# Performance work log

Hardware: AMD Instinct MI355X
Metric: run time of the kernel (lower is better)

Reference implementation:

```python
import jax, jax.numpy as jnp
import numpy as np

GAMMA = 2.0
CONTEXT_WINDOW = 100


def setup_inputs() -> dict:
    key = jax.random.key(0)
    k1, k2 = jax.random.split(key)
    B, S, C = 64, 131072, 3
    inputs = jax.random.normal(k1, (B, S, C), dtype=jnp.float32)
    targets = jax.random.randint(k2, (B, S), 0, C, dtype=jnp.int32)
    alpha = jnp.array([0.25, 1.0, 1.0], dtype=jnp.float32)
    return {"inputs": inputs, "targets": targets, "alpha": alpha}


def _window_mask(targets, window):
    # mask[b, i] = True iff any positive target within +/- window of i;
    # rows with no positives are fully True (matches torch loop semantics).
    B, S = targets.shape
    pos = targets > 0                                   # (B, S) bool
    cs = jnp.cumsum(pos.astype(jnp.int32), axis=1)      # inclusive prefix sums
    c = jnp.concatenate([jnp.zeros((B, 1), jnp.int32), cs], axis=1)  # (B, S+1)
    idx = jnp.arange(S)
    hi = jnp.minimum(idx + window + 1, S)               # exclusive end
    lo = jnp.maximum(idx - window, 0)                   # inclusive start
    count = c[:, hi] - c[:, lo]                         # positives in window
    mask = count > 0
    has_pos = pos.any(axis=1, keepdims=True)
    return jnp.where(has_pos, mask, True)


def reference(inputs, targets, alpha):
    # inputs: (B, S, C) logits; targets: (B, S) class indices
    mask = _window_mask(targets, CONTEXT_WINDOW)                     # (B, S)
    logp = jax.nn.log_softmax(inputs, axis=-1)                       # (B, S, C)
    ce = -jnp.take_along_axis(logp, targets[..., None].astype(jnp.int32), axis=-1)[..., 0]
    p_t = jnp.exp(-ce)
    focal = alpha[targets] * (1.0 - p_t) ** GAMMA * ce               # (B, S)
    m = mask.astype(inputs.dtype)
    # masked mean == mean over selected elements in the torch version
    return jnp.sum(focal * m) / jnp.sum(m)
```

## Files before the change

### kernel.cpp

```cpp
#include <hip/hip_runtime.h>

#define BB 64
#define SS 131072
#define CC 3
#define WIN 100
#define TILE 2048
#define NTHREADS 256
#define NBLOCKS (BB * (SS / TILE))
#define EXT (TILE + 2*WIN)
#define CHUNK ((EXT + NTHREADS - 1) / NTHREADS)

__global__ __launch_bounds__(NTHREADS) void focal_main(
    const float* __restrict__ inputs, const int* __restrict__ targets,
    const float* __restrict__ alpha, double* __restrict__ slots)
{
    __shared__ unsigned char sh_t[EXT];
    __shared__ int cs[EXT + 1];
    __shared__ int ssum[NTHREADS];
    __shared__ double red[(NTHREADS/64) * 3];

    const int t = threadIdx.x;
    const int b = blockIdx.x >> 6;
    const int tile = blockIdx.x & 63;
    const int s0 = tile * TILE;
    const int ext_lo = (s0 - WIN > 0) ? (s0 - WIN) : 0;
    const int ext_hi = (s0 + TILE + WIN < SS) ? (s0 + TILE + WIN) : SS;
    const int ext_len = ext_hi - ext_lo;

    const int* trow = targets + (long)b * SS;
    for (int k = t; k < ext_len; k += NTHREADS)
        sh_t[k] = (unsigned char)trow[ext_lo + k];
    __syncthreads();

    const int base = t * CHUNK;
    int lsum = 0;
    #pragma unroll
    for (int j = 0; j < CHUNK; ++j) {
        int idx = base + j;
        lsum += (idx < ext_len && sh_t[idx] > 0) ? 1 : 0;
    }
    ssum[t] = lsum;
    __syncthreads();
    #pragma unroll
    for (int off = 1; off < NTHREADS; off <<= 1) {
        int v = (t >= off) ? ssum[t - off] : 0;
        __syncthreads();
        ssum[t] += v;
        __syncthreads();
    }
    int run = ssum[t] - lsum;
    #pragma unroll
    for (int j = 0; j < CHUNK; ++j) {
        int idx = base + j;
        if (idx < ext_len) { cs[idx] = run; run += (sh_t[idx] > 0) ? 1 : 0; }
    }
    if (t == 0) cs[ext_len] = ssum[NTHREADS - 1];
    __syncthreads();

    const float a0 = alpha[0], a1 = alpha[1], a2 = alpha[2];
    const float* inrow = inputs + (long)b * SS * CC;
    float fsum_m = 0.0f, fsum_a = 0.0f;
    int cnt_m = 0;

    #pragma unroll
    for (int g = 0; g < TILE / (NTHREADS * 4); ++g) {
        const int p = s0 + (g * NTHREADS + t) * 4;
        const float4* ip = (const float4*)(inrow + (long)p * 3);
        float4 q0 = ip[0], q1 = ip[1], q2 = ip[2];
        float xs[12] = {q0.x, q0.y, q0.z, q0.w,
                        q1.x, q1.y, q1.z, q1.w,
                        q2.x, q2.y, q2.z, q2.w};
        #pragma unroll
        for (int j = 0; j < 4; ++j) {
            const int i = p + j;
            const float x0 = xs[3*j], x1 = xs[3*j+1], x2 = xs[3*j+2];
            const int tv = sh_t[i - ext_lo];
            const float mx = fmaxf(x0, fmaxf(x1, x2));
            const float e0 = __expf(x0 - mx), e1 = __expf(x1 - mx), e2 = __expf(x2 - mx);
            const float lse = mx + __logf(e0 + e1 + e2);
            const float xt = (tv == 0) ? x0 : ((tv == 1) ? x1 : x2);
            const float ce = lse - xt;
            const float pt = __expf(-ce);
            const float w  = (tv == 0) ? a0 : ((tv == 1) ? a1 : a2);
            const float om = 1.0f - pt;
            const float focal = w * om * om * ce;
            const int lo = (i - WIN > 0) ? (i - WIN) : 0;
            const int hi = (i + WIN + 1 < SS) ? (i + WIN + 1) : SS;
            const int cnt = cs[hi - ext_lo] - cs[lo - ext_lo];
            fsum_a += focal;
            if (cnt > 0) { fsum_m += focal; cnt_m += 1; }
        }
    }

    double dm = (double)fsum_m, da = (double)fsum_a, dc = (double)cnt_m;
    #pragma unroll
    for (int off = 32; off >= 1; off >>= 1) {
        dm += __shfl_down(dm, off);
        da += __shfl_down(da, off);
        dc += __shfl_down(dc, off);
    }
    const int wave = t >> 6, lane = t & 63;
    if (lane == 0) { red[wave*3] = dm; red[wave*3+1] = da; red[wave*3+2] = dc; }
    __syncthreads();
    if (t == 0) {
        double sm = 0, sa = 0, sc = 0;
        #pragma unroll
        for (int w = 0; w < NTHREADS/64; ++w) {
            sm += red[w*3]; sa += red[w*3+1]; sc += red[w*3+2];
        }
        const int te = (s0 + TILE < SS) ? (s0 + TILE) : SS;
        const int tile_cnt = cs[te - ext_lo] - cs[s0 - ext_lo];
        double* slot = slots + (long)blockIdx.x * 4;
        slot[0] = sm;
        slot[1] = sc;
        slot[2] = sa;
        slot[3] = (double)tile_cnt;
    }
}

__global__ __launch_bounds__(NTHREADS) void focal_final(
    const double* __restrict__ slots, float* __restrict__ out)
{
    __shared__ double red[(NTHREADS/64) * 2];
    __shared__ double tot[2];
    const int t = threadIdx.x;
    const int wave = t >> 6, lane = t & 63;

    double sm = 0.0, sc = 0.0;
    for (int k = t; k < NBLOCKS; k += NTHREADS) {
        sm += slots[(long)k * 4 + 0];
        sc += slots[(long)k * 4 + 1];
    }
    #pragma unroll
    for (int off = 32; off >= 1; off >>= 1) {
        sm += __shfl_down(sm, off);
        sc += __shfl_down(sc, off);
    }
    if (lane == 0) { red[wave*2] = sm; red[wave*2+1] = sc; }
    __syncthreads();
    if (t == 0) {
        double a = 0, b = 0;
        #pragma unroll
        for (int w = 0; w < NTHREADS/64; ++w) { a += red[w*2]; b += red[w*2+1]; }
        tot[0] = a; tot[1] = b;
    }
    __syncthreads();

    double corr_s = 0.0, corr_c = 0.0;
    if (t < BB) {
        double row_sum = 0.0, row_pos = 0.0;
        for (int j = 0; j < 64; ++j) {
            const long blk = (long)t * 64 + j;
            row_sum += slots[blk * 4 + 2];
            row_pos += slots[blk * 4 + 3];
        }
        if (row_pos == 0.0) { corr_s = row_sum; corr_c = (double)SS; }
    }
    if (wave == 0) {
        #pragma unroll
        for (int off = 32; off >= 1; off >>= 1) {
            corr_s += __shfl_down(corr_s, off);
            corr_c += __shfl_down(corr_c, off);
        }
        if (t == 0) {
            const double total = tot[0] + corr_s;
            const double count = tot[1] + corr_c;
            out[0] = (float)(total / count);
        }
    }
}

extern "C" void kernel_launch(void* const* d_in, const int* in_sizes, int n_in,
                              void* d_out, int out_size, void* d_ws, size_t ws_size,
                              hipStream_t stream) {
    const float* inputs  = (const float*)d_in[0];
    const int*   targets = (const int*)d_in[1];
    const float* alpha   = (const float*)d_in[2];
    float* out = (float*)d_out;

    double* slots = (double*)d_ws;

    focal_main<<<NBLOCKS, NTHREADS, 0, stream>>>(inputs, targets, alpha, slots);
    focal_final<<<1, NTHREADS, 0, stream>>>(slots, out);
}
```

Baseline: 181.9 us.

## Replace shared-memory prefix scan with wave ballot bitmasks for window mask

Drops the block-wide Hillis-Steele prefix sum over positives (many syncthreads) and instead builds a per-wave 64-bit ballot bitmap of positive targets, testing each window by OR-ing the masked words it covers. The logit float4 loads are issued at kernel start, before the target staging, so their latency overlaps the mask construction. The per-tile positive count now comes from per-element accumulation. The cost is a short variable-length loop over 3-5 shared words per element and more live registers.

New measurement: 184.2 us. Within noise of the previous version (+1.2%).

```diff
diff --git a/kernel.cpp b/kernel.cpp
--- a/kernel.cpp
+++ b/kernel.cpp
@@ -2,22 +2,21 @@
 
 #define BB 64
 #define SS 131072
-#define CC 3
 #define WIN 100
 #define TILE 2048
 #define NTHREADS 256
 #define NBLOCKS (BB * (SS / TILE))
 #define EXT (TILE + 2*WIN)
-#define CHUNK ((EXT + NTHREADS - 1) / NTHREADS)
+#define NITER ((EXT + NTHREADS - 1) / NTHREADS)
+#define NWORDS ((EXT + 63) / 64)
 
 __global__ __launch_bounds__(NTHREADS) void focal_main(
     const float* __restrict__ inputs, const int* __restrict__ targets,
     const float* __restrict__ alpha, double* __restrict__ slots)
 {
     __shared__ unsigned char sh_t[EXT];
-    __shared__ int cs[EXT + 1];
-    __shared__ int ssum[NTHREADS];
-    __shared__ double red[(NTHREADS/64) * 3];
+    __shared__ unsigned long long wbits[NWORDS];
+    __shared__ double red[(NTHREADS/64) * 4];
 
     const int t = threadIdx.x;
     const int b = blockIdx.x >> 6;
@@ -27,53 +26,47 @@
     const int ext_hi = (s0 + TILE + WIN < SS) ? (s0 + TILE + WIN) : SS;
     const int ext_len = ext_hi - ext_lo;
 
+    const float* inrow = inputs + (long)b * SS * 3;
+    const int p0 = s0 + t * 4;
+    const int p1 = s0 + (NTHREADS + t) * 4;
+    const float4* ip0 = (const float4*)(inrow + (long)p0 * 3);
+    const float4* ip1 = (const float4*)(inrow + (long)p1 * 3);
+    const float4 q0 = ip0[0], q1 = ip0[1], q2 = ip0[2];
+    const float4 q3 = ip1[0], q4 = ip1[1], q5 = ip1[2];
+
     const int* trow = targets + (long)b * SS;
-    for (int k = t; k < ext_len; k += NTHREADS)
-        sh_t[k] = (unsigned char)trow[ext_lo + k];
-    __syncthreads();
-
-    const int base = t * CHUNK;
-    int lsum = 0;
+    int tvv[NITER];
     #pragma unroll
-    for (int j = 0; j < CHUNK; ++j) {
-        int idx = base + j;
-        lsum += (idx < ext_len && sh_t[idx] > 0) ? 1 : 0;
+    for (int it = 0; it < NITER; ++it) {
+        const int k = it * NTHREADS + t;
+        tvv[it] = (k < ext_len) ? trow[ext_lo + k] : 0;
     }
-    ssum[t] = lsum;
-    __syncthreads();
+    const int wave = t >> 6, lane = t & 63;
     #pragma unroll
-    for (int off = 1; off < NTHREADS; off <<= 1) {
-        int v = (t >= off) ? ssum[t - off] : 0;
-        __syncthreads();
-        ssum[t] += v;
-        __syncthreads();
+    for (int it = 0; it < NITER; ++it) {
+        const int k = it * NTHREADS + t;
+        if (k < ext_len) sh_t[k] = (unsigned char)tvv[it];
+        const unsigned long long bal = __ballot(tvv[it] > 0);
+        if (lane == 0) wbits[it * 4 + wave] = bal;
     }
-    int run = ssum[t] - lsum;
-    #pragma unroll
-    for (int j = 0; j < CHUNK; ++j) {
-        int idx = base + j;
-        if (idx < ext_len) { cs[idx] = run; run += (sh_t[idx] > 0) ? 1 : 0; }
-    }
-    if (t == 0) cs[ext_len] = ssum[NTHREADS - 1];
     __syncthreads();
 
     const float a0 = alpha[0], a1 = alpha[1], a2 = alpha[2];
-    const float* inrow = inputs + (long)b * SS * CC;
     float fsum_m = 0.0f, fsum_a = 0.0f;
-    int cnt_m = 0;
+    int cnt_m = 0, cnt_p = 0;
+
+    const float xs[24] = {q0.x, q0.y, q0.z, q0.w, q1.x, q1.y, q1.z, q1.w,
+                          q2.x, q2.y, q2.z, q2.w, q3.x, q3.y, q3.z, q3.w,
+                          q4.x, q4.y, q4.z, q4.w, q5.x, q5.y, q5.z, q5.w};
 
     #pragma unroll
-    for (int g = 0; g < TILE / (NTHREADS * 4); ++g) {
-        const int p = s0 + (g * NTHREADS + t) * 4;
-        const float4* ip = (const float4*)(inrow + (long)p * 3);
-        float4 q0 = ip[0], q1 = ip[1], q2 = ip[2];
-        float xs[12] = {q0.x, q0.y, q0.z, q0.w,
-                        q1.x, q1.y, q1.z, q1.w,
-                        q2.x, q2.y, q2.z, q2.w};
+    for (int g = 0; g < 2; ++g) {
+        const int p = (g == 0) ? p0 : p1;
         #pragma unroll
         for (int j = 0; j < 4; ++j) {
             const int i = p + j;
-            const float x0 = xs[3*j], x1 = xs[3*j+1], x2 = xs[3*j+2];
+            const float x0 = xs[g*12 + 3*j], x1 = xs[g*12 + 3*j + 1],
+                        x2 = xs[g*12 + 3*j + 2];
             const int tv = sh_t[i - ext_lo];
             const float mx = fmaxf(x0, fmaxf(x1, x2));
             const float e0 = __expf(x0 - mx), e1 = __expf(x1 - mx), e2 = __expf(x2 - mx);
@@ -84,37 +77,52 @@
             const float w  = (tv == 0) ? a0 : ((tv == 1) ? a1 : a2);
             const float om = 1.0f - pt;
             const float focal = w * om * om * ce;
-            const int lo = (i - WIN > 0) ? (i - WIN) : 0;
-            const int hi = (i + WIN + 1 < SS) ? (i + WIN + 1) : SS;
-            const int cnt = cs[hi - ext_lo] - cs[lo - ext_lo];
+
+            int glo = i - WIN; if (glo < 0) glo = 0;
+            int ghi = i + WIN; if (ghi > SS - 1) ghi = SS - 1;
+            const int jlo = glo - ext_lo, jhi = ghi - ext_lo;
+            const int w0 = jlo >> 6, w1 = jhi >> 6;
+            unsigned long long acc = 0;
+            for (int wd = w0; wd <= w1; ++wd) {
+                unsigned long long v = wbits[wd];
+                if (wd == w0) v &= (~0ULL) << (jlo & 63);
+                if (wd == w1) v &= (~0ULL) >> (63 - (jhi & 63));
+                acc |= v;
+            }
+            const bool m = (acc != 0);
+
             fsum_a += focal;
-            if (cnt > 0) { fsum_m += focal; cnt_m += 1; }
+            fsum_m += m ? focal : 0.0f;
+            cnt_m += m ? 1 : 0;
+            cnt_p += (tv > 0) ? 1 : 0;
         }
     }
 
-    double dm = (double)fsum_m, da = (double)fsum_a, dc = (double)cnt_m;
+    double dm = (double)fsum_m, da = (double)fsum_a;
+    double dc = (double)cnt_m, dp = (double)cnt_p;
     #pragma unroll
     for (int off = 32; off >= 1; off >>= 1) {
         dm += __shfl_down(dm, off);
         da += __shfl_down(da, off);
         dc += __shfl_down(dc, off);
+        dp += __shfl_down(dp, off);
     }
-    const int wave = t >> 6, lane = t & 63;
-    if (lane == 0) { red[wave*3] = dm; red[wave*3+1] = da; red[wave*3+2] = dc; }
+    if (lane == 0) {
+        red[wave*4]   = dm; red[wave*4+1] = dc;
+        red[wave*4+2] = da; red[wave*4+3] = dp;
+    }
     __syncthreads();
     if (t == 0) {
-        double sm = 0, sa = 0, sc = 0;
+        double sm = 0, sc = 0, sa = 0, sp = 0;
         #pragma unroll
         for (int w = 0; w < NTHREADS/64; ++w) {
-            sm += red[w*3]; sa += red[w*3+1]; sc += red[w*3+2];
+            sm += red[w*4]; sc += red[w*4+1]; sa += red[w*4+2]; sp += red[w*4+3];
         }
-        const int te = (s0 + TILE < SS) ? (s0 + TILE) : SS;
-        const int tile_cnt = cs[te - ext_lo] - cs[s0 - ext_lo];
         double* slot = slots + (long)blockIdx.x * 4;
         slot[0] = sm;
         slot[1] = sc;
         slot[2] = sa;
-        slot[3] = (double)tile_cnt;
+        slot[3] = sp;
     }
 }
 
```
